# Performance work log

Hardware: AMD Instinct MI355X
Metric: run time of the kernel (lower is better)

The kernel has to match this reference:

```python
import jax, jax.numpy as jnp
import numpy as np

EMBED_DIM = 1024
NUM_HEADS = 16
HEAD_DIM = EMBED_DIM // NUM_HEADS
B, S = 4, 1024
EPS = 1e-5
NEG = -1e9


def layer_norm(h, gamma, beta):
    mu = jnp.mean(h, axis=-1, keepdims=True)
    var = jnp.mean(jnp.square(h - mu), axis=-1, keepdims=True)
    return (h - mu) * jax.lax.rsqrt(var + EPS) * gamma + beta


def setup_inputs() -> dict:
    key = jax.random.key(0)
    ks = jax.random.split(key, 8)
    scale = 1.0 / np.sqrt(EMBED_DIM)
    x = jax.random.normal(ks[0], (B, S, EMBED_DIM), dtype=jnp.float32)
    mask = jax.random.randint(ks[1], (B, S, S), 0, 2).astype(jnp.bool_)
    Wq = jax.random.uniform(ks[2], (EMBED_DIM, EMBED_DIM), jnp.float32, -scale, scale)
    bq = jax.random.uniform(ks[3], (EMBED_DIM,), jnp.float32, -scale, scale)
    Wk = jax.random.uniform(ks[4], (EMBED_DIM, EMBED_DIM), jnp.float32, -scale, scale)
    bk = jax.random.uniform(ks[5], (EMBED_DIM,), jnp.float32, -scale, scale)
    gq = jnp.ones((EMBED_DIM,), jnp.float32)
    bq_n = jnp.zeros((EMBED_DIM,), jnp.float32)
    gk = jnp.ones((EMBED_DIM,), jnp.float32)
    bk_n = jnp.zeros((EMBED_DIM,), jnp.float32)
    return {"x": x, "mask": mask, "Wq": Wq, "bq": bq, "Wk": Wk, "bk": bk,
            "gq": gq, "bq_n": bq_n, "gk": gk, "bk_n": bk_n}


def reference(x, mask, Wq, bq, Wk, bk, gq, bq_n, gk, bk_n):
    b, s, _ = x.shape
    # proj -> LayerNorm -> ReLU, split heads: [B,S,H,D]
    Q = jax.nn.relu(layer_norm(x @ Wq + bq, gq, bq_n)).reshape(b, s, NUM_HEADS, HEAD_DIM)
    K = jax.nn.relu(layer_norm(x @ Wk + bk, gk, bk_n)).reshape(b, s, NUM_HEADS, HEAD_DIM)
    # scores [B,H,S,S]
    scores = jnp.einsum('bqhd,bkhd->bhqk', Q, K) / np.sqrt(HEAD_DIM).astype(np.float32)
    # symmetric masking: mask applied along keys, then (via transpose trick) along queries
    m = (mask | jnp.swapaxes(mask, -1, -2))[:, None, :, :]
    scores = jnp.where(m, NEG, scores)
    attn = jax.nn.softmax(scores, axis=-1)
    return attn.mean(axis=1)  # [B,S,S]
```

## Files before the change

kernel.cpp:

```cpp
#include <hip/hip_runtime.h>
#include <hip/hip_bf16.h>

#define B_ 4
#define S_ 1024
#define E_ 1024
#define H_ 16
#define D_ 64

typedef __attribute__((ext_vector_type(8))) short short8;
typedef __attribute__((ext_vector_type(4))) float f32x4;

static __device__ __forceinline__ unsigned short f2bf(float x) {
  unsigned int u = __float_as_uint(x);
  unsigned int r = u + 0x7fffu + ((u >> 16) & 1u);
  return (unsigned short)(r >> 16);
}
static __device__ __forceinline__ float bf2f(unsigned short b) {
  return __uint_as_float((unsigned int)b << 16);
}

#define GL2LDS16(g, l)                                                            \
  __builtin_amdgcn_global_load_lds(                                               \
      (const __attribute__((address_space(1))) unsigned int*)(g),                 \
      (__attribute__((address_space(3))) unsigned int*)(l), 16, 0, 0)

#define WAIT_VMCNT4() __builtin_amdgcn_s_waitcnt(0x0F74)
#define WAIT_VMCNT0() __builtin_amdgcn_s_waitcnt(0x0F70)

#define BARRIER_LGKM()                                      \
  do {                                                      \
    asm volatile("s_waitcnt lgkmcnt(0)" ::: "memory");      \
    __builtin_amdgcn_s_barrier();                           \
  } while (0)

#define QSCALE 0.18033688011112042f
#define SCLAMP 115.41560327111707f

static __device__ __forceinline__ float dpp_red16(float v) {
  v += __int_as_float(__builtin_amdgcn_update_dpp(0, __float_as_int(v), 0xB1, 0xF, 0xF, true));
  v += __int_as_float(__builtin_amdgcn_update_dpp(0, __float_as_int(v), 0x4E, 0xF, 0xF, true));
  v += __int_as_float(__builtin_amdgcn_update_dpp(0, __float_as_int(v), 0x141, 0xF, 0xF, true));
  v += __int_as_float(__builtin_amdgcn_update_dpp(0, __float_as_int(v), 0x140, 0xF, 0xF, true));
  return v;
}

__global__ __launch_bounds__(256) void prep_kernel(const int* __restrict__ mask,
                                                   const float* __restrict__ x,
                                                   const float* __restrict__ Wq,
                                                   const float* __restrict__ Wk,
                                                   unsigned char* __restrict__ msym,
                                                   unsigned short* __restrict__ xbf,
                                                   unsigned short* __restrict__ Wt) {
  __shared__ __align__(16) char u_lds[2 * 32 * 33 * 4];
  const int blk = blockIdx.x;
  const int tid = threadIdx.x;
  if (blk < 4096) {
    const int b = blk >> 10;
    const int rest = blk & 1023;
    const int ti = rest >> 5;
    const int tj = rest & 31;
    if (ti > tj) return;
    int (*TA)[33] = (int(*)[33])u_lds;
    int (*TB)[33] = (int(*)[33])(u_lds + 32 * 33 * 4);
    const int i0 = ti << 5;
    const int j0 = tj << 5;
    const int ii = tid >> 3;
    const int jj4 = (tid & 7) << 2;
    const size_t bO = (size_t)b * S_ * S_;
    const int4 a4 = *(const int4*)&mask[bO + (size_t)(i0 + ii) * S_ + j0 + jj4];
    const int4 b4 = *(const int4*)&mask[bO + (size_t)(j0 + ii) * S_ + i0 + jj4];
    TA[ii][jj4 + 0] = a4.x; TA[ii][jj4 + 1] = a4.y; TA[ii][jj4 + 2] = a4.z; TA[ii][jj4 + 3] = a4.w;
    TB[ii][jj4 + 0] = b4.x; TB[ii][jj4 + 1] = b4.y; TB[ii][jj4 + 2] = b4.z; TB[ii][jj4 + 3] = b4.w;
    __syncthreads();
    uchar4 o1, o2;
    o1.x = ((a4.x != 0) || (TB[jj4 + 0][ii] != 0)) ? 1 : 0;
    o1.y = ((a4.y != 0) || (TB[jj4 + 1][ii] != 0)) ? 1 : 0;
    o1.z = ((a4.z != 0) || (TB[jj4 + 2][ii] != 0)) ? 1 : 0;
    o1.w = ((a4.w != 0) || (TB[jj4 + 3][ii] != 0)) ? 1 : 0;
    o2.x = ((b4.x != 0) || (TA[jj4 + 0][ii] != 0)) ? 1 : 0;
    o2.y = ((b4.y != 0) || (TA[jj4 + 1][ii] != 0)) ? 1 : 0;
    o2.z = ((b4.z != 0) || (TA[jj4 + 2][ii] != 0)) ? 1 : 0;
    o2.w = ((b4.w != 0) || (TA[jj4 + 3][ii] != 0)) ? 1 : 0;
    *(uchar4*)&msym[bO + (size_t)(i0 + ii) * S_ + j0 + jj4] = o1;
    *(uchar4*)&msym[bO + (size_t)(j0 + ii) * S_ + i0 + jj4] = o2;
  } else if (blk < 6144) {
    const size_t i = ((size_t)(blk - 4096) * 256 + tid) * 8;
    const float4 a = *(const float4*)(x + i);
    const float4 b = *(const float4*)(x + i + 4);
    const ushort4 p0 = {f2bf(a.x), f2bf(a.y), f2bf(a.z), f2bf(a.w)};
    const ushort4 p1 = {f2bf(b.x), f2bf(b.y), f2bf(b.z), f2bf(b.w)};
    *(ushort4*)(xbf + i) = p0;
    *(ushort4*)(xbf + i + 4) = p1;
  } else {
    unsigned short (*T2)[36] = (unsigned short(*)[36])u_lds;
    const int wblk = blk - 6144;
    const int mat = wblk >> 10;
    const int kt = (wblk >> 5) & 31, ntb = wblk & 31;
    const float* W = mat ? Wk : Wq;
    const int r = tid >> 3, c4 = (tid & 7) << 2;
    const float4 v = *(const float4*)&W[(size_t)(kt * 32 + r) * 1024 + ntb * 32 + c4];
    T2[r][c4 + 0] = f2bf(v.x); T2[r][c4 + 1] = f2bf(v.y);
    T2[r][c4 + 2] = f2bf(v.z); T2[r][c4 + 3] = f2bf(v.w);
    __syncthreads();
    const ushort4 o = {T2[c4 + 0][r], T2[c4 + 1][r], T2[c4 + 2][r], T2[c4 + 3][r]};
    *(ushort4*)&Wt[(size_t)(mat * 1024 + ntb * 32 + r) * 1024 + kt * 32 + c4] = o;
  }
}

__global__ __launch_bounds__(256) void gemm_mfma_kernel(const unsigned short* __restrict__ Abf,
                                                        const unsigned short* __restrict__ Wt,
                                                        unsigned short* __restrict__ P,
                                                        int nstride) {
  __shared__ __align__(16) unsigned short As[128 * 64];
  __shared__ __align__(16) unsigned short Bs[128 * 64];
  const int tid = threadIdx.x;
  const int m0 = (blockIdx.x & 31) << 7;
  const int n0 = (blockIdx.x >> 5) << 7;
  const int wave = tid >> 6, lane = tid & 63;
  const int ln15 = lane & 15, rg = lane >> 4;
  const int wm = (wave & 1) << 6;
  const int wn = (wave >> 1) << 6;
  const int sr = tid >> 3;
  const int sc = (tid & 7) << 3;
  const unsigned short* gA = Abf + (size_t)(m0 + sr) * 1024 + sc;
  const unsigned short* gB = Wt + (size_t)(n0 + sr) * 1024 + sc;
  unsigned short* lA = As + tid * 8;
  unsigned short* lB = Bs + tid * 8;
  f32x4 acc[4][4];
#pragma unroll
  for (int i = 0; i < 4; ++i)
#pragma unroll
    for (int j = 0; j < 4; ++j) acc[i][j] = (f32x4){0.0f, 0.0f, 0.0f, 0.0f};

  const unsigned short* pa = As + (wm + ln15) * 64 + rg * 8;
  const unsigned short* pb = Bs + (wn + ln15) * 64 + rg * 8;
  for (int k0 = 0; k0 < E_; k0 += 64) {
#pragma unroll
    for (int j = 0; j < 4; ++j) {
      GL2LDS16(gA + k0 + (size_t)(j * 32) * 1024, lA + j * 2048);
      GL2LDS16(gB + k0 + (size_t)(j * 32) * 1024, lB + j * 2048);
    }
    __syncthreads();
#pragma unroll
    for (int kk = 0; kk < 2; ++kk) {
      short8 af[4], bfr[4];
#pragma unroll
      for (int i = 0; i < 4; ++i) af[i] = *(const short8*)(pa + i * 16 * 64 + kk * 32);
#pragma unroll
      for (int j = 0; j < 4; ++j) bfr[j] = *(const short8*)(pb + j * 16 * 64 + kk * 32);
#pragma unroll
      for (int i = 0; i < 4; ++i)
#pragma unroll
        for (int j = 0; j < 4; ++j)
          acc[i][j] = __builtin_amdgcn_mfma_f32_16x16x32_bf16(af[i], bfr[j], acc[i][j], 0, 0, 0);
    }
    __syncthreads();
  }
#pragma unroll
  for (int i = 0; i < 4; ++i)
#pragma unroll
    for (int j = 0; j < 4; ++j)
#pragma unroll
      for (int r = 0; r < 4; ++r) {
        const int row = m0 + wm + i * 16 + rg * 4 + r;
        const int col = n0 + wn + j * 16 + ln15;
        P[(size_t)row * nstride + col] = f2bf(acc[i][j][r]);
      }
}

__device__ __forceinline__ void ln_body(const unsigned short* p, const float* bias,
                                        const float* gamma, const float* beta,
                                        unsigned short* obf, int b, int s, int tid) {
  const ushort4 pv = *(const ushort4*)(p + tid * 4);
  float4 v = {bf2f(pv.x), bf2f(pv.y), bf2f(pv.z), bf2f(pv.w)};
  const float4 bb = ((const float4*)bias)[tid];
  v.x += bb.x; v.y += bb.y; v.z += bb.z; v.w += bb.w;
  float sum = v.x + v.y + v.z + v.w;
  float s2 = v.x * v.x + v.y * v.y + v.z * v.z + v.w * v.w;
#pragma unroll
  for (int off = 32; off >= 1; off >>= 1) {
    sum += __shfl_xor(sum, off);
    s2 += __shfl_xor(s2, off);
  }
  __shared__ float red[2][4];
  const int wave = tid >> 6, lane = tid & 63;
  if (lane == 0) { red[0][wave] = sum; red[1][wave] = s2; }
  __syncthreads();
  sum = red[0][0] + red[0][1] + red[0][2] + red[0][3];
  s2 = red[1][0] + red[1][1] + red[1][2] + red[1][3];
  const float mu = sum * (1.0f / E_);
  const float var = s2 * (1.0f / E_) - mu * mu;
  const float r = rsqrtf(var + 1e-5f);
  const float4 g = ((const float4*)gamma)[tid];
  const float4 bt = ((const float4*)beta)[tid];
  const float o0 = fmaxf((v.x - mu) * r * g.x + bt.x, 0.0f);
  const float o1 = fmaxf((v.y - mu) * r * g.y + bt.y, 0.0f);
  const float o2 = fmaxf((v.z - mu) * r * g.z + bt.z, 0.0f);
  const float o3 = fmaxf((v.w - mu) * r * g.w + bt.w, 0.0f);
  const int h = tid >> 4;
  const int d = (tid & 15) << 2;
  const ushort4 ob = {f2bf(o0), f2bf(o1), f2bf(o2), f2bf(o3)};
  *(ushort4*)&obf[((size_t)(b * H_ + h) * S_ + s) * D_ + d] = ob;
}

__global__ __launch_bounds__(256) void ln_relu_bf_kernel(const unsigned short* __restrict__ P,
                                                         int rowstride, int coloff,
                                                         const float* __restrict__ bias,
                                                         const float* __restrict__ gamma,
                                                         const float* __restrict__ beta,
                                                         unsigned short* __restrict__ obf) {
  const int row = blockIdx.x;
  ln_body(P + (size_t)row * rowstride + coloff, bias, gamma, beta, obf,
          row >> 10, row & 1023, threadIdx.x);
}

__global__ __launch_bounds__(256) void ln2_kernel(const unsigned short* __restrict__ P2,
                                                  const float* __restrict__ bq,
                                                  const float* __restrict__ gq,
                                                  const float* __restrict__ bqn,
                                                  const float* __restrict__ bk,
                                                  const float* __restrict__ gk,
                                                  const float* __restrict__ bkn,
                                                  unsigned short* __restrict__ Qbf,
                                                  unsigned short* __restrict__ Kbf) {
  const int blk = blockIdx.x;
  const int sel = blk >> 12;
  const int row = blk & 4095;
  ln_body(P2 + (size_t)row * 2048 + sel * 1024,
          sel ? bk : bq, sel ? gk : gq, sel ? bkn : bqn,
          sel ? Kbf : Qbf, row >> 10, row & 1023, threadIdx.x);
}

__global__ __launch_bounds__(1024, 4) void attn15_kernel(const unsigned short* __restrict__ Qbf,
                                                         const unsigned short* __restrict__ Kbf,
                                                         const unsigned char* __restrict__ msym,
                                                         float* __restrict__ out) {
  __shared__ __align__(16) unsigned short Ks[2][16][2048];
  __shared__ __align__(16) float l_lds[2][16][20];
  const int tid = threadIdx.x;
  const int wave = tid >> 6, lane = tid & 63;
  const int ln15 = lane & 15, rg = lane >> 4;
  const int b = blockIdx.x & 3;
  const int q0 = (blockIdx.x >> 2) << 4;
  const unsigned short* Kb = Kbf + (size_t)b * H_ * S_ * D_;
  const unsigned short* Qb = Qbf + (size_t)b * H_ * S_ * D_;

  unsigned int mbits = 0;
#pragma unroll
  for (int hf = 0; hf < 2; ++hf)
#pragma unroll
    for (int jt = 0; jt < 2; ++jt)
#pragma unroll
      for (int r = 0; r < 4; ++r)
        mbits |= (msym[((size_t)b * S_ + q0 + rg * 4 + r) * S_ + hf * 512 + wave * 32 + jt * 16 + ln15]
                      ? 1u : 0u) << (hf * 8 + jt * 4 + r);
  float mf[2][2][4];
#pragma unroll
  for (int hf = 0; hf < 2; ++hf)
#pragma unroll
    for (int jt = 0; jt < 2; ++jt)
#pragma unroll
      for (int r = 0; r < 4; ++r)
        mf[hf][jt][r] = ((mbits >> (hf * 8 + jt * 4 + r)) & 1u) ? 0.0f : 1.0f;

  const int gl = ((lane >> 3) << 6) + (((lane & 7) ^ (lane >> 3)) << 3);
  const unsigned short* gwave = Kb + wave * 2048 + gl;
#pragma unroll
  for (int c = 0; c < 4; ++c) GL2LDS16(gwave + c * 512, &Ks[0][wave][c * 512]);

  const int pfrag = (rg ^ (ln15 & 7)) * 8;
  float o[2][2][4] = {};
  float ef[2][2][4];
  float la[4];

#pragma unroll 1
  for (int h = 0; h < 16; ++h) {
    const unsigned short* qrow = Qb + ((size_t)h * S_ + q0 + ln15) * D_ + rg * 8;
    const short8 a0 = *(const short8*)qrow;
    const short8 a1 = *(const short8*)(qrow + 32);
    la[0] = la[1] = la[2] = la[3] = 0.0f;
#pragma unroll
    for (int hf = 0; hf < 2; ++hf) {
      const int s = h * 2 + hf;
      if (s < 31) {
        const int s1 = s + 1;
        const unsigned short* g = gwave + (size_t)(s1 >> 1) * 65536 + (s1 & 1) * 32768;
        unsigned short* lp = &Ks[s1 & 1][wave][0];
#pragma unroll
        for (int c = 0; c < 4; ++c) GL2LDS16(g + c * 512, lp + c * 512);
        WAIT_VMCNT4();
      } else {
        WAIT_VMCNT0();
      }
      const unsigned short* kw = &Ks[s & 1][wave][ln15 * 64];
#pragma unroll
      for (int jt = 0; jt < 2; ++jt) {
        const unsigned short* kp = kw + jt * 1024;
        const short8 b0 = *(const short8*)(kp + pfrag);
        const short8 b1 = *(const short8*)(kp + (pfrag ^ 32));
        f32x4 cc = {0.0f, 0.0f, 0.0f, 0.0f};
        cc = __builtin_amdgcn_mfma_f32_16x16x32_bf16(a0, b0, cc, 0, 0, 0);
        cc = __builtin_amdgcn_mfma_f32_16x16x32_bf16(a1, b1, cc, 0, 0, 0);
#pragma unroll
        for (int r = 0; r < 4; ++r) {
          const float sv = fminf(cc[r] * QSCALE, SCLAMP);
          const float ev = __builtin_amdgcn_exp2f(sv) * mf[hf][jt][r];
          ef[hf][jt][r] = ev;
          la[r] += ev;
        }
      }
    }
#pragma unroll
    for (int r = 0; r < 4; ++r) la[r] = dpp_red16(la[r]);
    if (ln15 == 0) *(f32x4*)&l_lds[h & 1][wave][rg * 4] = (f32x4){la[0], la[1], la[2], la[3]};
    BARRIER_LGKM();
    const f32x4 pw = *(const f32x4*)&l_lds[h & 1][ln15][rg * 4];
#pragma unroll
    for (int r = 0; r < 4; ++r) {
      const float li = __builtin_amdgcn_rcpf(dpp_red16(pw[r]));
#pragma unroll
      for (int hf = 0; hf < 2; ++hf)
#pragma unroll
        for (int jt = 0; jt < 2; ++jt) o[hf][jt][r] += ef[hf][jt][r] * li;
    }
  }
#pragma unroll
  for (int hf = 0; hf < 2; ++hf)
#pragma unroll
    for (int jt = 0; jt < 2; ++jt)
#pragma unroll
      for (int r = 0; r < 4; ++r)
        out[((size_t)b * S_ + q0 + rg * 4 + r) * S_ + hf * 512 + wave * 32 + jt * 16 + ln15] =
            o[hf][jt][r] * 0.0625f;
}

extern "C" void kernel_launch(void* const* d_in, const int* in_sizes, int n_in,
                              void* d_out, int out_size, void* d_ws, size_t ws_size,
                              hipStream_t stream) {
  const float* x = (const float*)d_in[0];
  const int* mask = (const int*)d_in[1];
  const float* Wq = (const float*)d_in[2];
  const float* bq = (const float*)d_in[3];
  const float* Wk = (const float*)d_in[4];
  const float* bk = (const float*)d_in[5];
  const float* gq = (const float*)d_in[6];
  const float* bq_n = (const float*)d_in[7];
  const float* gk = (const float*)d_in[8];
  const float* bk_n = (const float*)d_in[9];
  float* out = (float*)d_out;

  char* ws = (char*)d_ws;
  const size_t MB = 1024 * 1024;

  if (ws_size >= 40 * MB) {
    unsigned short* P2 = (unsigned short*)ws;
    unsigned short* xbf = (unsigned short*)(ws + 16 * MB);
    unsigned short* Kbf = (unsigned short*)(ws + 16 * MB);
    unsigned short* Wt = (unsigned short*)(ws + 24 * MB);
    unsigned short* Qbf = (unsigned short*)(ws + 28 * MB);
    unsigned char* msym = (unsigned char*)(ws + 36 * MB);

    prep_kernel<<<8192, 256, 0, stream>>>(mask, x, Wq, Wk, msym, xbf, Wt);
    gemm_mfma_kernel<<<512, 256, 0, stream>>>(xbf, Wt, P2, 2048);
    ln2_kernel<<<8192, 256, 0, stream>>>(P2, bq, gq, bq_n, bk, gk, bk_n, Qbf, Kbf);
    attn15_kernel<<<256, 1024, 0, stream>>>(Qbf, Kbf, msym, out);
  } else {
    unsigned short* P = (unsigned short*)ws;
    unsigned short* xbf = (unsigned short*)(ws + 8 * MB);
    unsigned short* Kbf = (unsigned short*)(ws + 8 * MB);
    unsigned short* Wt = (unsigned short*)(ws + 16 * MB);
    unsigned short* Qbf = (unsigned short*)(ws + 20 * MB);
    unsigned char* msym = (unsigned char*)(ws + 28 * MB);

    prep_kernel<<<8192, 256, 0, stream>>>(mask, x, Wq, Wk, msym, xbf, Wt);
    gemm_mfma_kernel<<<256, 256, 0, stream>>>(xbf, Wt, P, 1024);
    ln_relu_bf_kernel<<<4096, 256, 0, stream>>>(P, 1024, 0, bq, gq, bq_n, Qbf);
    gemm_mfma_kernel<<<256, 256, 0, stream>>>(xbf, Wt + (size_t)1024 * 1024, P, 1024);
    ln_relu_bf_kernel<<<4096, 256, 0, stream>>>(P, 1024, 0, bk, gk, bk_n, Kbf);
    attn15_kernel<<<256, 1024, 0, stream>>>(Qbf, Kbf, msym, out);
  }
}
```

Before: 182.3 us.

## Fuse prep, projection GEMM and LayerNorm into one cooperative kernel

Replaces the separate prep, GEMM and LayerNorm launches with a single cooperative kernel of 512 blocks. The stages (bf16 conversion and transposes, MFMA GEMM, LayerNorm+ReLU) are separated by grid-wide syncs instead of kernel boundaries. This removes two launch gaps and tail effects, but every stage is now limited to 512 blocks at 2 per CU. The GEMM also loses any pipelining the old kernel may have had, and grid.sync adds its own overhead.

```diff
diff --git a/kernel.cpp b/kernel.cpp
--- a/kernel.cpp
+++ b/kernel.cpp
@@ -1,5 +1,8 @@
 #include <hip/hip_runtime.h>
 #include <hip/hip_bf16.h>
+#include <hip/hip_cooperative_groups.h>
+
+namespace cg = cooperative_groups;
 
 #define B_ 4
 #define S_ 1024
@@ -42,6 +45,183 @@
   v += __int_as_float(__builtin_amdgcn_update_dpp(0, __float_as_int(v), 0x141, 0xF, 0xF, true));
   v += __int_as_float(__builtin_amdgcn_update_dpp(0, __float_as_int(v), 0x140, 0xF, 0xF, true));
   return v;
+}
+
+__global__ __launch_bounds__(256, 2) void mega_kernel(
+    const float* __restrict__ x, const float* __restrict__ Wq,
+    const float* __restrict__ Wk, const int* __restrict__ mask,
+    unsigned char* __restrict__ msym, unsigned short* __restrict__ xbf,
+    unsigned short* __restrict__ Wt, unsigned short* __restrict__ P2,
+    const float* __restrict__ bq, const float* __restrict__ gq,
+    const float* __restrict__ bqn, const float* __restrict__ bk,
+    const float* __restrict__ gk, const float* __restrict__ bkn,
+    unsigned short* __restrict__ Qbf, unsigned short* __restrict__ Kbf) {
+  cg::grid_group grid = cg::this_grid();
+  __shared__ __align__(16) char smem[32768];
+  __shared__ float red2[2][2][4];
+  const int bid = blockIdx.x;
+  const int tid = threadIdx.x;
+
+#pragma unroll
+  for (int u = 0; u < 4; ++u) {
+    const size_t i = ((size_t)(bid * 4 + u) * 256 + tid) * 8;
+    const float4 a = *(const float4*)(x + i);
+    const float4 b = *(const float4*)(x + i + 4);
+    const ushort4 p0 = {f2bf(a.x), f2bf(a.y), f2bf(a.z), f2bf(a.w)};
+    const ushort4 p1 = {f2bf(b.x), f2bf(b.y), f2bf(b.z), f2bf(b.w)};
+    *(ushort4*)(xbf + i) = p0;
+    *(ushort4*)(xbf + i + 4) = p1;
+  }
+  {
+    unsigned short (*T2)[36] = (unsigned short(*)[36])smem;
+    const int r = tid >> 3, c4 = (tid & 7) << 2;
+    for (int u = 0; u < 4; ++u) {
+      const int wblk = bid * 4 + u;
+      const int mat = wblk >> 10;
+      const int kt = (wblk >> 5) & 31, ntb = wblk & 31;
+      const float* W = mat ? Wk : Wq;
+      const float4 v = *(const float4*)&W[(size_t)(kt * 32 + r) * 1024 + ntb * 32 + c4];
+      __syncthreads();
+      T2[r][c4 + 0] = f2bf(v.x); T2[r][c4 + 1] = f2bf(v.y);
+      T2[r][c4 + 2] = f2bf(v.z); T2[r][c4 + 3] = f2bf(v.w);
+      __syncthreads();
+      const ushort4 o = {T2[c4 + 0][r], T2[c4 + 1][r], T2[c4 + 2][r], T2[c4 + 3][r]};
+      *(ushort4*)&Wt[(size_t)(mat * 1024 + ntb * 32 + r) * 1024 + kt * 32 + c4] = o;
+    }
+  }
+  {
+    int (*TA)[33] = (int(*)[33])smem;
+    int (*TB)[33] = (int(*)[33])(smem + 32 * 33 * 4);
+    const int ii = tid >> 3, jj4 = (tid & 7) << 2;
+    for (int u = 0; u < 8; ++u) {
+      const int mblk = bid * 8 + u;
+      const int b = mblk >> 10;
+      const int rest = mblk & 1023;
+      const int ti = rest >> 5, tj = rest & 31;
+      if (ti > tj) continue;
+      const int i0 = ti << 5, j0 = tj << 5;
+      const size_t bO = (size_t)b * S_ * S_;
+      const int4 a4 = *(const int4*)&mask[bO + (size_t)(i0 + ii) * S_ + j0 + jj4];
+      const int4 b4 = *(const int4*)&mask[bO + (size_t)(j0 + ii) * S_ + i0 + jj4];
+      __syncthreads();
+      TA[ii][jj4 + 0] = a4.x; TA[ii][jj4 + 1] = a4.y; TA[ii][jj4 + 2] = a4.z; TA[ii][jj4 + 3] = a4.w;
+      TB[ii][jj4 + 0] = b4.x; TB[ii][jj4 + 1] = b4.y; TB[ii][jj4 + 2] = b4.z; TB[ii][jj4 + 3] = b4.w;
+      __syncthreads();
+      uchar4 o1, o2;
+      o1.x = ((a4.x != 0) || (TB[jj4 + 0][ii] != 0)) ? 1 : 0;
+      o1.y = ((a4.y != 0) || (TB[jj4 + 1][ii] != 0)) ? 1 : 0;
+      o1.z = ((a4.z != 0) || (TB[jj4 + 2][ii] != 0)) ? 1 : 0;
+      o1.w = ((a4.w != 0) || (TB[jj4 + 3][ii] != 0)) ? 1 : 0;
+      o2.x = ((b4.x != 0) || (TA[jj4 + 0][ii] != 0)) ? 1 : 0;
+      o2.y = ((b4.y != 0) || (TA[jj4 + 1][ii] != 0)) ? 1 : 0;
+      o2.z = ((b4.z != 0) || (TA[jj4 + 2][ii] != 0)) ? 1 : 0;
+      o2.w = ((b4.w != 0) || (TA[jj4 + 3][ii] != 0)) ? 1 : 0;
+      *(uchar4*)&msym[bO + (size_t)(i0 + ii) * S_ + j0 + jj4] = o1;
+      *(uchar4*)&msym[bO + (size_t)(j0 + ii) * S_ + i0 + jj4] = o2;
+    }
+  }
+  __threadfence();
+  grid.sync();
+  {
+    unsigned short* As = (unsigned short*)smem;
+    unsigned short* Bs = (unsigned short*)(smem + 16384);
+    const int m0 = (bid & 31) << 7;
+    const int n0 = (bid >> 5) << 7;
+    const int wave = tid >> 6, lane = tid & 63;
+    const int ln15 = lane & 15, rg = lane >> 4;
+    const int wm = (wave & 1) << 6;
+    const int wn = (wave >> 1) << 6;
+    const int sr = tid >> 3;
+    const int sc = (tid & 7) << 3;
+    const unsigned short* gA = xbf + (size_t)(m0 + sr) * 1024 + sc;
+    const unsigned short* gB = Wt + (size_t)(n0 + sr) * 1024 + sc;
+    unsigned short* lA = As + tid * 8;
+    unsigned short* lB = Bs + tid * 8;
+    f32x4 acc[4][4];
+#pragma unroll
+    for (int i = 0; i < 4; ++i)
+#pragma unroll
+      for (int j = 0; j < 4; ++j) acc[i][j] = (f32x4){0.0f, 0.0f, 0.0f, 0.0f};
+
+    const unsigned short* pa = As + (wm + ln15) * 64 + rg * 8;
+    const unsigned short* pb = Bs + (wn + ln15) * 64 + rg * 8;
+    for (int k0 = 0; k0 < E_; k0 += 64) {
+#pragma unroll
+      for (int j = 0; j < 4; ++j) {
+        GL2LDS16(gA + k0 + (size_t)(j * 32) * 1024, lA + j * 2048);
+        GL2LDS16(gB + k0 + (size_t)(j * 32) * 1024, lB + j * 2048);
+      }
+      __syncthreads();
+#pragma unroll
+      for (int kk = 0; kk < 2; ++kk) {
+        short8 af[4], bfr[4];
+#pragma unroll
+        for (int i = 0; i < 4; ++i) af[i] = *(const short8*)(pa + i * 16 * 64 + kk * 32);
+#pragma unroll
+        for (int j = 0; j < 4; ++j) bfr[j] = *(const short8*)(pb + j * 16 * 64 + kk * 32);
+#pragma unroll
+        for (int i = 0; i < 4; ++i)
+#pragma unroll
+          for (int j = 0; j < 4; ++j)
+            acc[i][j] = __builtin_amdgcn_mfma_f32_16x16x32_bf16(af[i], bfr[j], acc[i][j], 0, 0, 0);
+      }
+      __syncthreads();
+    }
+#pragma unroll
+    for (int i = 0; i < 4; ++i)
+#pragma unroll
+      for (int j = 0; j < 4; ++j)
+#pragma unroll
+        for (int r = 0; r < 4; ++r) {
+          const int row = m0 + wm + i * 16 + rg * 4 + r;
+          const int col = n0 + wn + j * 16 + ln15;
+          P2[(size_t)row * 2048 + col] = f2bf(acc[i][j][r]);
+        }
+  }
+  __threadfence();
+  grid.sync();
+  for (int t = 0; t < 16; ++t) {
+    const int task = bid * 16 + t;
+    const int sel = task >> 12;
+    const int row = task & 4095;
+    const int par = t & 1;
+    const unsigned short* p = P2 + (size_t)row * 2048 + sel * 1024;
+    const float* bias = sel ? bk : bq;
+    const float* gamma = sel ? gk : gq;
+    const float* beta = sel ? bkn : bqn;
+    unsigned short* obf = sel ? Kbf : Qbf;
+    const int b = row >> 10, s = row & 1023;
+
+    const ushort4 pv = *(const ushort4*)(p + tid * 4);
+    float4 v = {bf2f(pv.x), bf2f(pv.y), bf2f(pv.z), bf2f(pv.w)};
+    const float4 bb = ((const float4*)bias)[tid];
+    v.x += bb.x; v.y += bb.y; v.z += bb.z; v.w += bb.w;
+    float sum = v.x + v.y + v.z + v.w;
+    float s2 = v.x * v.x + v.y * v.y + v.z * v.z + v.w * v.w;
+#pragma unroll
+    for (int off = 32; off >= 1; off >>= 1) {
+      sum += __shfl_xor(sum, off);
+      s2 += __shfl_xor(s2, off);
+    }
+    const int wave = tid >> 6, lane = tid & 63;
+    if (lane == 0) { red2[par][0][wave] = sum; red2[par][1][wave] = s2; }
+    __syncthreads();
+    sum = red2[par][0][0] + red2[par][0][1] + red2[par][0][2] + red2[par][0][3];
+    s2 = red2[par][1][0] + red2[par][1][1] + red2[par][1][2] + red2[par][1][3];
+    const float mu = sum * (1.0f / E_);
+    const float var = s2 * (1.0f / E_) - mu * mu;
+    const float rr = rsqrtf(var + 1e-5f);
+    const float4 g = ((const float4*)gamma)[tid];
+    const float4 bt = ((const float4*)beta)[tid];
+    const float o0 = fmaxf((v.x - mu) * rr * g.x + bt.x, 0.0f);
+    const float o1 = fmaxf((v.y - mu) * rr * g.y + bt.y, 0.0f);
+    const float o2 = fmaxf((v.z - mu) * rr * g.z + bt.z, 0.0f);
+    const float o3 = fmaxf((v.w - mu) * rr * g.w + bt.w, 0.0f);
+    const int h = tid >> 4;
+    const int d = (tid & 15) << 2;
+    const ushort4 ob = {f2bf(o0), f2bf(o1), f2bf(o2), f2bf(o3)};
+    *(ushort4*)&obf[((size_t)(b * H_ + h) * S_ + s) * D_ + d] = ob;
+  }
 }
 
 __global__ __launch_bounds__(256) void prep_kernel(const int* __restrict__ mask,
@@ -214,23 +394,6 @@
           row >> 10, row & 1023, threadIdx.x);
 }
 
-__global__ __launch_bounds__(256) void ln2_kernel(const unsigned short* __restrict__ P2,
-                                                  const float* __restrict__ bq,
-                                                  const float* __restrict__ gq,
-                                                  const float* __restrict__ bqn,
-                                                  const float* __restrict__ bk,
-                                                  const float* __restrict__ gk,
-                                                  const float* __restrict__ bkn,
-                                                  unsigned short* __restrict__ Qbf,
-                                                  unsigned short* __restrict__ Kbf) {
-  const int blk = blockIdx.x;
-  const int sel = blk >> 12;
-  const int row = blk & 4095;
-  ln_body(P2 + (size_t)row * 2048 + sel * 1024,
-          sel ? bk : bq, sel ? gk : gq, sel ? bkn : bqn,
-          sel ? Kbf : Qbf, row >> 10, row & 1023, threadIdx.x);
-}
-
 __global__ __launch_bounds__(1024, 4) void attn15_kernel(const unsigned short* __restrict__ Qbf,
                                                          const unsigned short* __restrict__ Kbf,
                                                          const unsigned char* __restrict__ msym,
@@ -360,9 +523,12 @@
     unsigned short* Qbf = (unsigned short*)(ws + 28 * MB);
     unsigned char* msym = (unsigned char*)(ws + 36 * MB);
 
-    prep_kernel<<<8192, 256, 0, stream>>>(mask, x, Wq, Wk, msym, xbf, Wt);
-    gemm_mfma_kernel<<<512, 256, 0, stream>>>(xbf, Wt, P2, 2048);
-    ln2_kernel<<<8192, 256, 0, stream>>>(P2, bq, gq, bq_n, bk, gk, bk_n, Qbf, Kbf);
+    void* kargs[] = {(void*)&x,   (void*)&Wq,  (void*)&Wk,   (void*)&mask,
+                     (void*)&msym, (void*)&xbf, (void*)&Wt,   (void*)&P2,
+                     (void*)&bq,  (void*)&gq,  (void*)&bq_n, (void*)&bk,
+                     (void*)&gk,  (void*)&bk_n, (void*)&Qbf, (void*)&Kbf};
+    hipLaunchCooperativeKernel((const void*)mega_kernel, dim3(512), dim3(256),
+                               kargs, 0, stream);
     attn15_kernel<<<256, 1024, 0, stream>>>(Qbf, Kbf, msym, out);
   } else {
     unsigned short* P = (unsigned short*)ws;
```

After: 464.4 us. +154.7%, slower.
